# Kernel optimization log

Measured on AMD Instinct MI355X. Metric: run time of the kernel, lower is better.

## Reference

```python
import jax, jax.numpy as jnp
import numpy as np

D_MODEL = 1024
NUM_HEADS = 16
HEAD_DIM = D_MODEL // NUM_HEADS
THETA = 10000.0
B, S = 4, 2048


def _rope(x, pos):
    # x: [B, H, S, d], pos: [B, S] int
    half = HEAD_DIM // 2
    inv_freq = THETA ** (-(jnp.arange(half, dtype=jnp.float32) * 2.0) / HEAD_DIM)  # [half]
    ang = pos.astype(jnp.float32)[:, None, :, None] * inv_freq  # [B, 1, S, half]
    cos, sin = jnp.cos(ang), jnp.sin(ang)
    x1, x2 = x[..., 0::2], x[..., 1::2]  # interleaved pairs
    r1 = x1 * cos - x2 * sin
    r2 = x1 * sin + x2 * cos
    return jnp.stack([r1, r2], axis=-1).reshape(x.shape)


def setup_inputs() -> dict:
    key = jax.random.key(0)
    ks = jax.random.split(key, 12)
    scale = 1.0 / np.sqrt(D_MODEL)
    inp = {
        "query": jax.random.normal(ks[0], (B, S, D_MODEL), dtype=jnp.float32),
        "key": jax.random.normal(ks[1], (B, S, D_MODEL), dtype=jnp.float32),
        "value": jax.random.normal(ks[2], (B, S, D_MODEL), dtype=jnp.float32),
        "token_positions": jnp.broadcast_to(jnp.arange(S, dtype=jnp.int32), (B, S)),
        "w_q": jax.random.normal(ks[3], (D_MODEL, D_MODEL), dtype=jnp.float32) * scale,
        "b_q": jnp.zeros((D_MODEL,), dtype=jnp.float32),
        "w_k": jax.random.normal(ks[4], (D_MODEL, D_MODEL), dtype=jnp.float32) * scale,
        "b_k": jnp.zeros((D_MODEL,), dtype=jnp.float32),
        "w_v": jax.random.normal(ks[5], (D_MODEL, D_MODEL), dtype=jnp.float32) * scale,
        "b_v": jnp.zeros((D_MODEL,), dtype=jnp.float32),
        "w_o": jax.random.normal(ks[6], (D_MODEL, D_MODEL), dtype=jnp.float32) * scale,
        "b_o": jnp.zeros((D_MODEL,), dtype=jnp.float32),
    }
    return inp


def reference(query, key, value, token_positions, w_q, b_q, w_k, b_k, w_v, b_v, w_o, b_o):
    b, s, _ = query.shape
    Q = query @ w_q + b_q
    K = key @ w_k + b_k
    V = value @ w_v + b_v
    # [B, S, H, d] -> [B, H, S, d]
    Q = Q.reshape(b, s, NUM_HEADS, HEAD_DIM).transpose(0, 2, 1, 3)
    K = K.reshape(b, s, NUM_HEADS, HEAD_DIM).transpose(0, 2, 1, 3)
    V = V.reshape(b, s, NUM_HEADS, HEAD_DIM).transpose(0, 2, 1, 3)
    Q = _rope(Q, token_positions)
    K = _rope(K, token_positions)
    scores = jnp.einsum("bhqd,bhkd->bhqk", Q, K) / jnp.sqrt(jnp.float32(HEAD_DIM))
    causal = jnp.tril(jnp.ones((s, s), dtype=bool))
    scores = jnp.where(causal, scores, -jnp.inf)
    attn = jax.nn.softmax(scores, axis=-1)
    out = jnp.einsum("bhqk,bhkd->bhqd", attn, V)
    out = out.transpose(0, 2, 1, 3).reshape(b, s, D_MODEL)
    return out @ w_o + b_o
```

## Files before the change

### kernel.cpp

```cpp
#include <hip/hip_runtime.h>

typedef __bf16 bf16;
typedef __attribute__((ext_vector_type(8))) __bf16 bf16x8;
typedef __attribute__((ext_vector_type(4))) __bf16 bf16x4;
typedef __attribute__((ext_vector_type(4))) float floatx4;

#define MFMA16(a, b, c) __builtin_amdgcn_mfma_f32_16x16x32_bf16((a), (b), (c), 0, 0, 0)

#define GLL(g, l)                                                   \
  __builtin_amdgcn_global_load_lds(                                 \
      (const __attribute__((address_space(1))) void*)(g),           \
      (__attribute__((address_space(3))) void*)(l), 16, 0, 0)

static constexpr int DM = 1024;
static constexpr int SEQ = 2048;
static constexpr int BATCH = 4;
static constexpr int NH = 16;
static constexpr int HD = 64;
static constexpr float LOG2E = 1.4426950408889634f;
static constexpr float LOG2_THETA = 13.287712379549449f;

__global__ __launch_bounds__(256) void convert_x(
    const float* __restrict__ q, const float* __restrict__ k,
    const float* __restrict__ v, bf16* __restrict__ qo,
    bf16* __restrict__ ko, bf16* __restrict__ vo) {
  int z = blockIdx.z;
  const float* src = (z == 0) ? q : (z == 1) ? k : v;
  bf16* dst = (z == 0) ? qo : (z == 1) ? ko : vo;
  size_t i = ((size_t)blockIdx.x * blockDim.x + threadIdx.x) * 8;
  float4 a = *(const float4*)(src + i);
  float4 b = *(const float4*)(src + i + 4);
  bf16x8 o;
  o[0] = (bf16)a.x; o[1] = (bf16)a.y; o[2] = (bf16)a.z; o[3] = (bf16)a.w;
  o[4] = (bf16)b.x; o[5] = (bf16)b.y; o[6] = (bf16)b.z; o[7] = (bf16)b.w;
  *(bf16x8*)(dst + i) = o;
}

__global__ __launch_bounds__(256) void convert_w(
    const float* __restrict__ wq, const float* __restrict__ wk,
    const float* __restrict__ wv, const float* __restrict__ wo,
    bf16* __restrict__ oq, bf16* __restrict__ ok, bf16* __restrict__ ov,
    bf16* __restrict__ oo) {
  int z = blockIdx.z;
  const float* src = (z == 0) ? wq : (z == 1) ? wk : (z == 2) ? wv : wo;
  bf16* dst = (z == 0) ? oq : (z == 1) ? ok : (z == 2) ? ov : oo;
  __shared__ __align__(16) bf16 T[64][72];
  int k0 = blockIdx.y * 64, n0 = blockIdx.x * 64;
  int tid = threadIdx.x;
  int r = tid >> 4, c4 = (tid & 15) * 4;
#pragma unroll
  for (int i = 0; i < 4; i++) {
    int kk = r + i * 16;
    float4 v = *(const float4*)(src + (size_t)(k0 + kk) * DM + n0 + c4);
    T[c4 + 0][kk] = (bf16)v.x;
    T[c4 + 1][kk] = (bf16)v.y;
    T[c4 + 2][kk] = (bf16)v.z;
    T[c4 + 3][kk] = (bf16)v.w;
  }
  __syncthreads();
#pragma unroll
  for (int i = 0; i < 4; i++) {
    int nn = r + i * 16;
    bf16x4 o = *(const bf16x4*)&T[nn][c4];
    *(bf16x4*)(dst + (size_t)(n0 + nn) * DM + k0 + c4) = o;
  }
}

__global__ __launch_bounds__(256) void rope_table(const int* __restrict__ tp,
                                                  float* __restrict__ tab) {
  int idx = blockIdx.x * 256 + threadIdx.x;
  int m = idx >> 5, i = idx & 31;
  float pos = (float)tp[m];
  float invf = exp2f(-(float)(2 * i) * (LOG2_THETA / 64.0f));
  float s, c;
  sincosf(pos * invf, &s, &c);
  tab[(size_t)idx * 2] = c;
  tab[(size_t)idx * 2 + 1] = s;
}

__global__ __launch_bounds__(256) void gemm_qkv(
    const bf16* __restrict__ qb, const bf16* __restrict__ kb,
    const bf16* __restrict__ vb, const bf16* __restrict__ wqt,
    const bf16* __restrict__ wkt, const bf16* __restrict__ wvt,
    const float* __restrict__ biq, const float* __restrict__ bik,
    const float* __restrict__ biv, const float* __restrict__ tab,
    bf16* __restrict__ Qr, bf16* __restrict__ Kr, bf16* __restrict__ Vr) {
  int z = blockIdx.z;
  const bf16* X = (z == 0) ? qb : (z == 1) ? kb : vb;
  const bf16* Wt = (z == 0) ? wqt : (z == 1) ? wkt : wvt;
  const float* bias = (z == 0) ? biq : (z == 1) ? bik : biv;

  __shared__ __align__(16) bf16 As[128 * 32];
  __shared__ __align__(16) bf16 Bs[128 * 32];
  int tid = threadIdx.x;
  int lane = tid & 63, wv = tid >> 6;
  int quad = lane >> 4, low = lane & 15;
  int m0 = blockIdx.y * 128, n0 = blockIdx.x * 128;
  int wm = (wv >> 1) * 64, wn = (wv & 1) * 64;
  int lr = lane >> 2, lc = (lane & 3) * 8;
  const bf16* AgL = X + (size_t)(m0 + wv * 16 + lr) * DM + lc;
  const bf16* BgL = Wt + (size_t)(n0 + wv * 16 + lr) * DM + lc;
  bf16* AsL = As + wv * 512;
  bf16* BsL = Bs + wv * 512;

  floatx4 acc[4][4];
#pragma unroll
  for (int i = 0; i < 4; i++)
#pragma unroll
    for (int j = 0; j < 4; j++) acc[i][j] = (floatx4)0.0f;

  for (int kt = 0; kt < DM; kt += 32) {
    GLL(AgL + kt, AsL);
    GLL(AgL + kt + (size_t)64 * DM, AsL + 2048);
    GLL(BgL + kt, BsL);
    GLL(BgL + kt + (size_t)64 * DM, BsL + 2048);
    __syncthreads();
    bf16x8 af[4], bfr[4];
#pragma unroll
    for (int t = 0; t < 4; t++)
      af[t] = *(const bf16x8*)&As[(wm + t * 16 + low) * 32 + quad * 8];
#pragma unroll
    for (int t = 0; t < 4; t++)
      bfr[t] = *(const bf16x8*)&Bs[(wn + t * 16 + low) * 32 + quad * 8];
#pragma unroll
    for (int mt = 0; mt < 4; mt++)
#pragma unroll
      for (int nt = 0; nt < 4; nt++)
        acc[mt][nt] = MFMA16(af[mt], bfr[nt], acc[mt][nt]);
    __syncthreads();
  }

#pragma unroll
  for (int nt = 0; nt < 4; nt++) {
    int n = n0 + wn + nt * 16 + low;
    float bias_v = bias[n];
    int h = n >> 6, d = n & 63, di = d >> 1;
#pragma unroll
    for (int mt = 0; mt < 4; mt++) {
#pragma unroll
      for (int r = 0; r < 4; r++) {
        int m = m0 + wm + mt * 16 + quad * 4 + r;
        float val = acc[mt][nt][r] + bias_v;
        int bb = m >> 11, ss = m & 2047;
        if (z < 2) {
          float2 cs = *(const float2*)(tab + ((size_t)m * 32 + di) * 2);
          float pv = __shfl_xor(val, 1);
          float o = (d & 1) ? (pv * cs.y + val * cs.x)
                            : (val * cs.x - pv * cs.y);
          if (z == 0) o *= 0.125f * LOG2E;
          bf16* dst = (z == 0) ? Qr : Kr;
          dst[((size_t)(bb * NH + h) * SEQ + ss) * HD + d] = (bf16)o;
        } else {
          Vr[((size_t)(bb * NH + h) * SEQ + ss) * HD + d] = (bf16)val;
        }
      }
    }
  }
}

__global__ __launch_bounds__(256) void transpose_v(const bf16* __restrict__ Vr,
                                                   bf16* __restrict__ Vt) {
  int bh = blockIdx.y;
  int s0 = blockIdx.x * 64;
  __shared__ __align__(16) bf16 T[64][72];
  int t = threadIdx.x;
  int r = t >> 2, c = (t & 3) * 16;
  const bf16* src = Vr + ((size_t)bh * SEQ + s0 + r) * HD + c;
  bf16x8 a = *(const bf16x8*)src;
  bf16x8 b = *(const bf16x8*)(src + 8);
  *(bf16x8*)&T[r][c] = a;
  *(bf16x8*)&T[r][c + 8] = b;
  __syncthreads();
  bf16* dst = Vt + ((size_t)bh * HD + r) * SEQ + s0 + c;
  bf16x8 o0, o1;
#pragma unroll
  for (int j = 0; j < 8; j++) {
    o0[j] = T[c + j][r];
    o1[j] = T[c + 8 + j][r];
  }
  *(bf16x8*)dst = o0;
  *(bf16x8*)(dst + 8) = o1;
}

__global__ __launch_bounds__(256, 2) void attn_fa(const bf16* __restrict__ Qr,
                                                  const bf16* __restrict__ Kr,
                                                  const bf16* __restrict__ Vt,
                                                  bf16* __restrict__ attn) {
  int bh = blockIdx.y, bx = blockIdx.x;
  int tid = threadIdx.x, lane = tid & 63, w = tid >> 6;
  int quad = lane >> 4, low = lane & 15;
  __shared__ __align__(16) bf16 Ks[2][64 * 72];
  __shared__ __align__(16) bf16 Vs[2][64 * 72];
  __shared__ __align__(16) bf16 Pl[4][2][16 * 72];
  const bf16* Qh = Qr + (size_t)bh * SEQ * HD;
  const bf16* Kh = Kr + (size_t)bh * SEQ * HD;
  const bf16* Vh = Vt + (size_t)bh * HD * SEQ;
  int bb = bh >> 4, h = bh & 15;

  int sr = tid >> 2, scol = (tid & 3) * 16;
  const bf16* Kg = Kh + (size_t)sr * HD + scol;
  const bf16* Vg = Vh + (size_t)sr * SEQ + scol;
  int sl = sr * 72 + scol;

  bf16x8 ones;
#pragma unroll
  for (int j = 0; j < 8; j++) ones[j] = (bf16)1.0f;

  for (int pass = 0; pass < 2; pass++) {
    int qi = pass ? bx : (15 - bx);
    int ntiles = 2 * qi + 2;
    int qrow0 = qi * 128 + w * 32;

    bf16x8 aq[2][2];
#pragma unroll
    for (int rt = 0; rt < 2; rt++)
#pragma unroll
      for (int kc = 0; kc < 2; kc++)
        aq[rt][kc] = *(const bf16x8*)(Qh +
                                      (size_t)(qrow0 + rt * 16 + low) * HD +
                                      kc * 32 + quad * 8);

    floatx4 accO[2][4];
    floatx4 lacc[2];
#pragma unroll
    for (int rt = 0; rt < 2; rt++) {
      lacc[rt] = (floatx4)0.0f;
#pragma unroll
      for (int nt = 0; nt < 4; nt++) accO[rt][nt] = (floatx4)0.0f;
    }

    {
      bf16x8 k0 = *(const bf16x8*)(Kg);
      bf16x8 k1 = *(const bf16x8*)(Kg + 8);
      bf16x8 v0 = *(const bf16x8*)(Vg);
      bf16x8 v1 = *(const bf16x8*)(Vg + 8);
      *(bf16x8*)&Ks[0][sl] = k0;
      *(bf16x8*)&Ks[0][sl + 8] = k1;
      *(bf16x8*)&Vs[0][sl] = v0;
      *(bf16x8*)&Vs[0][sl + 8] = v1;
    }
    __syncthreads();

    for (int kt = 0; kt < ntiles; kt++) {
      int cur = kt & 1;
      bf16x8 nk0, nk1, nv0, nv1;
      bool pre = (kt + 1 < ntiles);
      if (pre) {
        const bf16* kg = Kg + (size_t)(kt + 1) * (64 * HD);
        const bf16* vg = Vg + (size_t)(kt + 1) * 64;
        nk0 = *(const bf16x8*)(kg);
        nk1 = *(const bf16x8*)(kg + 8);
        nv0 = *(const bf16x8*)(vg);
        nv1 = *(const bf16x8*)(vg + 8);
      }

      floatx4 s2[2][4];
#pragma unroll
      for (int rt = 0; rt < 2; rt++)
#pragma unroll
        for (int nt = 0; nt < 4; nt++) s2[rt][nt] = (floatx4)0.0f;
#pragma unroll
      for (int nt = 0; nt < 4; nt++) {
        bf16x8 kb0 = *(const bf16x8*)&Ks[cur][(nt * 16 + low) * 72 + quad * 8];
        bf16x8 kb1 =
            *(const bf16x8*)&Ks[cur][(nt * 16 + low) * 72 + 32 + quad * 8];
#pragma unroll
        for (int rt = 0; rt < 2; rt++) {
          s2[rt][nt] = MFMA16(kb0, aq[rt][0], s2[rt][nt]);
          s2[rt][nt] = MFMA16(kb1, aq[rt][1], s2[rt][nt]);
        }
      }
      if (kt >= ntiles - 2) {
#pragma unroll
        for (int nt = 0; nt < 4; nt++)
#pragma unroll
          for (int r = 0; r < 4; r++) {
            int kg_ = kt * 64 + nt * 16 + quad * 4 + r;
#pragma unroll
            for (int rt = 0; rt < 2; rt++) {
              int qg = qrow0 + rt * 16 + low;
              if (kg_ > qg) s2[rt][nt][r] = -INFINITY;
            }
          }
      }
#pragma unroll
      for (int rt = 0; rt < 2; rt++)
#pragma unroll
        for (int nt = 0; nt < 4; nt++) {
          bf16x4 pk;
#pragma unroll
          for (int r = 0; r < 4; r++) pk[r] = (bf16)exp2f(s2[rt][nt][r]);
          *(bf16x4*)&Pl[w][rt][low * 72 + nt * 16 + quad * 4] = pk;
        }
      bf16x8 vb0[4], vb1[4];
#pragma unroll
      for (int nt = 0; nt < 4; nt++) {
        vb0[nt] = *(const bf16x8*)&Vs[cur][(nt * 16 + low) * 72 + quad * 8];
        vb1[nt] =
            *(const bf16x8*)&Vs[cur][(nt * 16 + low) * 72 + 32 + quad * 8];
      }
      asm volatile("s_waitcnt lgkmcnt(0)" ::: "memory");
#pragma unroll
      for (int rt = 0; rt < 2; rt++) {
        bf16x8 ap0 = *(const bf16x8*)&Pl[w][rt][low * 72 + quad * 8];
        bf16x8 ap1 = *(const bf16x8*)&Pl[w][rt][low * 72 + 32 + quad * 8];
#pragma unroll
        for (int nt = 0; nt < 4; nt++) {
          accO[rt][nt] = MFMA16(ap0, vb0[nt], accO[rt][nt]);
          accO[rt][nt] = MFMA16(ap1, vb1[nt], accO[rt][nt]);
        }
        lacc[rt] = MFMA16(ap0, ones, lacc[rt]);
        lacc[rt] = MFMA16(ap1, ones, lacc[rt]);
      }
      if (pre) {
        int nb = cur ^ 1;
        *(bf16x8*)&Ks[nb][sl] = nk0;
        *(bf16x8*)&Ks[nb][sl + 8] = nk1;
        *(bf16x8*)&Vs[nb][sl] = nv0;
        *(bf16x8*)&Vs[nb][sl + 8] = nv1;
      }
      __syncthreads();
    }

#pragma unroll
    for (int rt = 0; rt < 2; rt++)
#pragma unroll
      for (int r = 0; r < 4; r++) {
        float inv = 1.0f / lacc[rt][r];
        int q = qrow0 + rt * 16 + quad * 4 + r;
#pragma unroll
        for (int nt = 0; nt < 4; nt++) {
          float o = accO[rt][nt][r] * inv;
          attn[((size_t)(bb * SEQ + q)) * DM + h * HD + nt * 16 + low] =
              (bf16)o;
        }
      }
  }
}

__global__ __launch_bounds__(256) void gemm_out(const bf16* __restrict__ X,
                                                const bf16* __restrict__ Wt,
                                                const float* __restrict__ bias,
                                                float* __restrict__ out) {
  __shared__ __align__(16) bf16 As[128 * 32];
  __shared__ __align__(16) bf16 Bs[128 * 32];
  int tid = threadIdx.x;
  int lane = tid & 63, wv = tid >> 6;
  int quad = lane >> 4, low = lane & 15;
  int m0 = blockIdx.y * 128, n0 = blockIdx.x * 128;
  int wm = (wv >> 1) * 64, wn = (wv & 1) * 64;
  int lr = lane >> 2, lc = (lane & 3) * 8;
  const bf16* AgL = X + (size_t)(m0 + wv * 16 + lr) * DM + lc;
  const bf16* BgL = Wt + (size_t)(n0 + wv * 16 + lr) * DM + lc;
  bf16* AsL = As + wv * 512;
  bf16* BsL = Bs + wv * 512;

  floatx4 acc[4][4];
#pragma unroll
  for (int i = 0; i < 4; i++)
#pragma unroll
    for (int j = 0; j < 4; j++) acc[i][j] = (floatx4)0.0f;

  for (int kt = 0; kt < DM; kt += 32) {
    GLL(AgL + kt, AsL);
    GLL(AgL + kt + (size_t)64 * DM, AsL + 2048);
    GLL(BgL + kt, BsL);
    GLL(BgL + kt + (size_t)64 * DM, BsL + 2048);
    __syncthreads();
    bf16x8 af[4], bfr[4];
#pragma unroll
    for (int t = 0; t < 4; t++)
      af[t] = *(const bf16x8*)&As[(wm + t * 16 + low) * 32 + quad * 8];
#pragma unroll
    for (int t = 0; t < 4; t++)
      bfr[t] = *(const bf16x8*)&Bs[(wn + t * 16 + low) * 32 + quad * 8];
#pragma unroll
    for (int mt = 0; mt < 4; mt++)
#pragma unroll
      for (int nt = 0; nt < 4; nt++)
        acc[mt][nt] = MFMA16(af[mt], bfr[nt], acc[mt][nt]);
    __syncthreads();
  }

#pragma unroll
  for (int nt = 0; nt < 4; nt++) {
    int n = n0 + wn + nt * 16 + low;
    float bias_v = bias[n];
#pragma unroll
    for (int mt = 0; mt < 4; mt++)
#pragma unroll
      for (int r = 0; r < 4; r++) {
        int m = m0 + wm + mt * 16 + quad * 4 + r;
        out[(size_t)m * DM + n] = acc[mt][nt][r] + bias_v;
      }
  }
}

extern "C" void kernel_launch(void* const* d_in, const int* in_sizes, int n_in,
                              void* d_out, int out_size, void* d_ws,
                              size_t ws_size, hipStream_t stream) {
  const float* query = (const float*)d_in[0];
  const float* key_ = (const float*)d_in[1];
  const float* value = (const float*)d_in[2];
  const int* tp = (const int*)d_in[3];
  const float* w_q = (const float*)d_in[4];
  const float* b_q = (const float*)d_in[5];
  const float* w_k = (const float*)d_in[6];
  const float* b_k = (const float*)d_in[7];
  const float* w_v = (const float*)d_in[8];
  const float* b_v = (const float*)d_in[9];
  const float* w_o = (const float*)d_in[10];
  const float* b_o = (const float*)d_in[11];

  char* w = (char*)d_ws;
  const size_t MB = 1u << 20;
  bf16* qb = (bf16*)(w + 0);
  bf16* kb = (bf16*)(w + 16 * MB);
  bf16* vb = (bf16*)(w + 32 * MB);
  bf16* wqt = (bf16*)(w + 48 * MB);
  bf16* wkt = (bf16*)(w + 50 * MB);
  bf16* wvt = (bf16*)(w + 52 * MB);
  bf16* wot = (bf16*)(w + 54 * MB);
  bf16* Qr = (bf16*)(w + 56 * MB);
  bf16* Kr = (bf16*)(w + 72 * MB);
  bf16* Vr = (bf16*)(w + 88 * MB);
  float* tab = (float*)(w + 104 * MB);
  bf16* Vt = (bf16*)(w + 32 * MB);
  bf16* attnb = (bf16*)(w + 0);

  convert_x<<<dim3(4096, 1, 3), 256, 0, stream>>>(query, key_, value, qb, kb,
                                                  vb);
  convert_w<<<dim3(16, 16, 4), 256, 0, stream>>>(w_q, w_k, w_v, w_o, wqt, wkt,
                                                 wvt, wot);
  rope_table<<<1024, 256, 0, stream>>>(tp, tab);
  gemm_qkv<<<dim3(8, 64, 3), 256, 0, stream>>>(qb, kb, vb, wqt, wkt, wvt, b_q,
                                               b_k, b_v, tab, Qr, Kr, Vr);
  transpose_v<<<dim3(32, 64), 256, 0, stream>>>(Vr, Vt);
  attn_fa<<<dim3(8, 64), 256, 0, stream>>>(Qr, Kr, Vt, attnb);
  gemm_out<<<dim3(8, 64), 256, 0, stream>>>(attnb, wot, b_o, (float*)d_out);
}
```

Before: 398.2 us.

## Swap MFMA operands for vectorized GEMM epilogues and linearize block grids

The QKV and output GEMMs now pass the weight tile as the first MFMA operand, so each lane's four accumulator values cover four consecutive output columns. This lets the epilogues do one float4 bias load, an in-register RoPE pair rotation with a float4 table read, and 8-byte bf16x4 or 16-byte float4 stores in place of scattered scalar stores and lane shuffles. The grids of the two GEMMs and the attention kernel are also flattened to 1D with the M or head index varying fastest. That changes which blocks run together, which may improve L2 reuse of weight tiles but also reorders the causal-attention work across heads and query blocks.

Result: faster. 353.5 us (-11.2%).

```diff
diff --git a/kernel.cpp b/kernel.cpp
--- a/kernel.cpp
+++ b/kernel.cpp
@@ -19,6 +19,7 @@
 static constexpr int HD = 64;
 static constexpr float LOG2E = 1.4426950408889634f;
 static constexpr float LOG2_THETA = 13.287712379549449f;
+static constexpr float QSC = 0.125f * LOG2E;
 
 __global__ __launch_bounds__(256) void convert_x(
     const float* __restrict__ q, const float* __restrict__ k,
@@ -92,10 +93,11 @@
 
   __shared__ __align__(16) bf16 As[128 * 32];
   __shared__ __align__(16) bf16 Bs[128 * 32];
+  int lin = blockIdx.x;
+  int m0 = (lin & 63) * 128, n0 = (lin >> 6) * 128;
   int tid = threadIdx.x;
   int lane = tid & 63, wv = tid >> 6;
   int quad = lane >> 4, low = lane & 15;
-  int m0 = blockIdx.y * 128, n0 = blockIdx.x * 128;
   int wm = (wv >> 1) * 64, wn = (wv & 1) * 64;
   int lr = lane >> 2, lc = (lane & 3) * 8;
   const bf16* AgL = X + (size_t)(m0 + wv * 16 + lr) * DM + lc;
@@ -115,44 +117,51 @@
     GLL(BgL + kt, BsL);
     GLL(BgL + kt + (size_t)64 * DM, BsL + 2048);
     __syncthreads();
-    bf16x8 af[4], bfr[4];
+    bf16x8 xf[4], wf[4];
 #pragma unroll
     for (int t = 0; t < 4; t++)
-      af[t] = *(const bf16x8*)&As[(wm + t * 16 + low) * 32 + quad * 8];
+      xf[t] = *(const bf16x8*)&As[(wm + t * 16 + low) * 32 + quad * 8];
 #pragma unroll
     for (int t = 0; t < 4; t++)
-      bfr[t] = *(const bf16x8*)&Bs[(wn + t * 16 + low) * 32 + quad * 8];
-#pragma unroll
-    for (int mt = 0; mt < 4; mt++)
-#pragma unroll
-      for (int nt = 0; nt < 4; nt++)
-        acc[mt][nt] = MFMA16(af[mt], bfr[nt], acc[mt][nt]);
+      wf[t] = *(const bf16x8*)&Bs[(wn + t * 16 + low) * 32 + quad * 8];
+#pragma unroll
+    for (int i = 0; i < 4; i++)
+#pragma unroll
+      for (int j = 0; j < 4; j++)
+        acc[i][j] = MFMA16(wf[i], xf[j], acc[i][j]);
     __syncthreads();
   }
 
 #pragma unroll
-  for (int nt = 0; nt < 4; nt++) {
-    int n = n0 + wn + nt * 16 + low;
-    float bias_v = bias[n];
-    int h = n >> 6, d = n & 63, di = d >> 1;
-#pragma unroll
-    for (int mt = 0; mt < 4; mt++) {
-#pragma unroll
-      for (int r = 0; r < 4; r++) {
-        int m = m0 + wm + mt * 16 + quad * 4 + r;
-        float val = acc[mt][nt][r] + bias_v;
-        int bb = m >> 11, ss = m & 2047;
-        if (z < 2) {
-          float2 cs = *(const float2*)(tab + ((size_t)m * 32 + di) * 2);
-          float pv = __shfl_xor(val, 1);
-          float o = (d & 1) ? (pv * cs.y + val * cs.x)
-                            : (val * cs.x - pv * cs.y);
-          if (z == 0) o *= 0.125f * LOG2E;
-          bf16* dst = (z == 0) ? Qr : Kr;
-          dst[((size_t)(bb * NH + h) * SEQ + ss) * HD + d] = (bf16)o;
-        } else {
-          Vr[((size_t)(bb * NH + h) * SEQ + ss) * HD + d] = (bf16)val;
-        }
+  for (int i = 0; i < 4; i++) {
+    int nb = n0 + wn + i * 16 + quad * 4;
+    float4 bv = *(const float4*)(bias + nb);
+    int h = nb >> 6, dbase = nb & 63;
+#pragma unroll
+    for (int j = 0; j < 4; j++) {
+      int m = m0 + wm + j * 16 + low;
+      int bb = m >> 11, ss = m & 2047;
+      float v0 = acc[i][j][0] + bv.x;
+      float v1 = acc[i][j][1] + bv.y;
+      float v2 = acc[i][j][2] + bv.z;
+      float v3 = acc[i][j][3] + bv.w;
+      size_t off = ((size_t)(bb * NH + h) * SEQ + ss) * HD + dbase;
+      bf16x4 pk;
+      if (z < 2) {
+        float4 cs = *(const float4*)(tab + (size_t)m * 64 + dbase);
+        float o0 = v0 * cs.x - v1 * cs.y;
+        float o1 = v0 * cs.y + v1 * cs.x;
+        float o2 = v2 * cs.z - v3 * cs.w;
+        float o3 = v2 * cs.w + v3 * cs.z;
+        if (z == 0) { o0 *= QSC; o1 *= QSC; o2 *= QSC; o3 *= QSC; }
+        pk[0] = (bf16)o0; pk[1] = (bf16)o1;
+        pk[2] = (bf16)o2; pk[3] = (bf16)o3;
+        bf16* dst = (z == 0) ? Qr : Kr;
+        *(bf16x4*)(dst + off) = pk;
+      } else {
+        pk[0] = (bf16)v0; pk[1] = (bf16)v1;
+        pk[2] = (bf16)v2; pk[3] = (bf16)v3;
+        *(bf16x4*)(Vr + off) = pk;
       }
     }
   }
@@ -186,7 +195,8 @@
                                                   const bf16* __restrict__ Kr,
                                                   const bf16* __restrict__ Vt,
                                                   bf16* __restrict__ attn) {
-  int bh = blockIdx.y, bx = blockIdx.x;
+  int lin = blockIdx.x;
+  int bh = lin & 63, bx = lin >> 6;
   int tid = threadIdx.x, lane = tid & 63, w = tid >> 6;
   int quad = lane >> 4, low = lane & 15;
   __shared__ __align__(16) bf16 Ks[2][64 * 72];
@@ -344,10 +354,11 @@
                                                 float* __restrict__ out) {
   __shared__ __align__(16) bf16 As[128 * 32];
   __shared__ __align__(16) bf16 Bs[128 * 32];
+  int lin = blockIdx.x;
+  int m0 = (lin & 63) * 128, n0 = (lin >> 6) * 128;
   int tid = threadIdx.x;
   int lane = tid & 63, wv = tid >> 6;
   int quad = lane >> 4, low = lane & 15;
-  int m0 = blockIdx.y * 128, n0 = blockIdx.x * 128;
   int wm = (wv >> 1) * 64, wn = (wv & 1) * 64;
   int lr = lane >> 2, lc = (lane & 3) * 8;
   const bf16* AgL = X + (size_t)(m0 + wv * 16 + lr) * DM + lc;
@@ -367,32 +378,35 @@
     GLL(BgL + kt, BsL);
     GLL(BgL + kt + (size_t)64 * DM, BsL + 2048);
     __syncthreads();
-    bf16x8 af[4], bfr[4];
+    bf16x8 xf[4], wf[4];
 #pragma unroll
     for (int t = 0; t < 4; t++)
-      af[t] = *(const bf16x8*)&As[(wm + t * 16 + low) * 32 + quad * 8];
+      xf[t] = *(const bf16x8*)&As[(wm + t * 16 + low) * 32 + quad * 8];
 #pragma unroll
     for (int t = 0; t < 4; t++)
-      bfr[t] = *(const bf16x8*)&Bs[(wn + t * 16 + low) * 32 + quad * 8];
-#pragma unroll
-    for (int mt = 0; mt < 4; mt++)
-#pragma unroll
-      for (int nt = 0; nt < 4; nt++)
-        acc[mt][nt] = MFMA16(af[mt], bfr[nt], acc[mt][nt]);
+      wf[t] = *(const bf16x8*)&Bs[(wn + t * 16 + low) * 32 + quad * 8];
+#pragma unroll
+    for (int i = 0; i < 4; i++)
+#pragma unroll
+      for (int j = 0; j < 4; j++)
+        acc[i][j] = MFMA16(wf[i], xf[j], acc[i][j]);
     __syncthreads();
   }
 
 #pragma unroll
-  for (int nt = 0; nt < 4; nt++) {
-    int n = n0 + wn + nt * 16 + low;
-    float bias_v = bias[n];
-#pragma unroll
-    for (int mt = 0; mt < 4; mt++)
-#pragma unroll
-      for (int r = 0; r < 4; r++) {
-        int m = m0 + wm + mt * 16 + quad * 4 + r;
-        out[(size_t)m * DM + n] = acc[mt][nt][r] + bias_v;
-      }
+  for (int i = 0; i < 4; i++) {
+    int nb = n0 + wn + i * 16 + quad * 4;
+    float4 bv = *(const float4*)(bias + nb);
+#pragma unroll
+    for (int j = 0; j < 4; j++) {
+      int m = m0 + wm + j * 16 + low;
+      float4 o;
+      o.x = acc[i][j][0] + bv.x;
+      o.y = acc[i][j][1] + bv.y;
+      o.z = acc[i][j][2] + bv.z;
+      o.w = acc[i][j][3] + bv.w;
+      *(float4*)(out + (size_t)m * DM + nb) = o;
+    }
   }
 }
 
@@ -433,9 +447,10 @@
   convert_w<<<dim3(16, 16, 4), 256, 0, stream>>>(w_q, w_k, w_v, w_o, wqt, wkt,
                                                  wvt, wot);
   rope_table<<<1024, 256, 0, stream>>>(tp, tab);
-  gemm_qkv<<<dim3(8, 64, 3), 256, 0, stream>>>(qb, kb, vb, wqt, wkt, wvt, b_q,
-                                               b_k, b_v, tab, Qr, Kr, Vr);
+  gemm_qkv<<<dim3(512, 1, 3), 256, 0, stream>>>(qb, kb, vb, wqt, wkt, wvt,
+                                                b_q, b_k, b_v, tab, Qr, Kr,
+                                                Vr);
   transpose_v<<<dim3(32, 64), 256, 0, stream>>>(Vr, Vt);
-  attn_fa<<<dim3(8, 64), 256, 0, stream>>>(Qr, Kr, Vt, attnb);
-  gemm_out<<<dim3(8, 64), 256, 0, stream>>>(attnb, wot, b_o, (float*)d_out);
-}
+  attn_fa<<<dim3(512), 256, 0, stream>>>(Qr, Kr, Vt, attnb);
+  gemm_out<<<dim3(512), 256, 0, stream>>>(attnb, wot, b_o, (float*)d_out);
+}
```
